# Optimization experiments

Hardware: AMD Instinct MI355X
Metric: run time of the kernel (lower is better)

Reference implementation:

```python
import jax, jax.numpy as jnp
from jax import lax
import numpy as np

B, T, K = 256, 512, 256
MAX_SEQ = 512  # max_sequence_length; output padded to MAX_SEQ + 2


def setup_inputs() -> dict:
    key = jax.random.key(0)
    k1, k2 = jax.random.split(key)
    emissions = jax.random.normal(k1, (B, T, K), dtype=jnp.float32)
    transitions = jax.random.normal(k2, (K, K), dtype=jnp.float32)
    mask = jnp.ones((B, T), dtype=jnp.int32)  # prefix mask; here full-length
    return {"emissions": emissions, "transitions": transitions, "mask": mask,
            "max_sequence_length": MAX_SEQ}


def _crf_decode(emissions, transitions, mask):
    # emissions: [B, T, K] float; transitions: [K, K]; mask: [B, T] int (prefix 1s)
    b, t, k = emissions.shape
    state0 = emissions[:, 0, :]                      # [B, K]
    em_rest = jnp.swapaxes(emissions[:, 1:, :], 0, 1)  # [T-1, B, K]
    mk_rest = jnp.swapaxes(mask[:, 1:], 0, 1)           # [T-1, B]

    def fwd(state, xs):
        em_t, mk_t = xs
        # scores[b, i, j] = state[b, i] + transitions[i, j]  (prev tag i -> cur tag j)
        scores = state[:, :, None] + transitions[None, :, :]   # [B, K, K]
        bp = jnp.argmax(scores, axis=1).astype(jnp.int32)       # [B, K] best prev tag
        new_state = jnp.max(scores, axis=1) + em_t              # [B, K]
        valid = (mk_t > 0)[:, None]
        # RNN-with-mask semantics: keep last valid state past sequence end
        return jnp.where(valid, new_state, state), bp

    last_state, bps = lax.scan(fwd, state0, (em_rest, mk_rest))  # bps: [T-1, B, K]
    last_tag = jnp.argmax(last_state, axis=-1).astype(jnp.int32)  # [B]

    def bwd(tag, xs):
        bp_t, mk_t = xs
        out = tag  # tag at this timestep
        prev = jnp.take_along_axis(bp_t, tag[:, None], axis=1)[:, 0]
        tag = jnp.where(mk_t > 0, prev, tag)  # only step back on valid positions
        return tag, out

    tag0, outs = lax.scan(bwd, last_tag, (bps, mk_rest), reverse=True)
    # outs[t] = tag at position t+1 (t = 0..T-2); tag0 = tag at position 0
    tags = jnp.concatenate([tag0[:, None], jnp.swapaxes(outs, 0, 1)], axis=1)  # [B, T]
    return tags


def reference(emissions, transitions, mask, max_sequence_length):
    tags = _crf_decode(emissions, transitions, mask)
    tags = tags * mask  # zero out padding positions
    pad = max_sequence_length + 2 - tags.shape[1]
    return jnp.pad(tags, ((0, 0), (0, pad)))
```

## Files before the change

kernel.cpp:

```cpp
#include <hip/hip_runtime.h>


#define TK 256
#define TT 512

typedef float v2f __attribute__((ext_vector_type(2)));

__global__ void transpose_kernel(const float* __restrict__ trans,
                                 float* __restrict__ transT) {
  int j = blockIdx.x;
  int i = threadIdx.x;
  transT[(size_t)j * TK + i] = trans[(size_t)i * TK + j];
}

__global__ __launch_bounds__(1024, 4) void crf_fwd(const float* __restrict__ em,
                                                   const float* __restrict__ trans,
                                                   const int* __restrict__ mask,
                                                   float* __restrict__ states) {
  const int b = blockIdx.x;
  const int tid = threadIdx.x;
  const int j = tid & (TK - 1);
  const int h = tid >> 8;

  __shared__ __align__(16) float st[TK];
  __shared__ float part[3 * TK];
  __shared__ int mk[TT];

  v2f tr2[32];
#pragma unroll
  for (int i = 0; i < 32; ++i) {
    tr2[i].x = trans[(size_t)(h * 64 + 2 * i + 0) * TK + j];
    tr2[i].y = trans[(size_t)(h * 64 + 2 * i + 1) * TK + j];
  }

  if (tid < TT) mk[tid] = mask[(size_t)b * TT + tid];

  const size_t base = (size_t)b * TT * TK;
  float cur = 0.f;
  if (h == 0) {
    cur = em[base + j];
    st[j] = cur;
    states[base + j] = cur;
  }
  __syncthreads();

  const float* stp = st + h * 64;
  const float* emp = em + base + TK + j;
  float* outp = states + base + TK + j;

  for (int t = 1; t < TT; ++t) {
    float emv = 0.f;
    if (h == 0) emv = *emp;

    float m0 = -INFINITY, m1 = -INFINITY;
#pragma unroll
    for (int k = 0; k < 16; ++k) {
      const float4 s4 = *reinterpret_cast<const float4*>(stp + 4 * k);
      v2f a = {s4.x, s4.y};
      v2f c = {s4.z, s4.w};
      a = a + tr2[2 * k + 0];
      c = c + tr2[2 * k + 1];
      m0 = fmaxf(fmaxf(m0, a.x), a.y);
      m1 = fmaxf(fmaxf(m1, c.x), c.y);
    }
    const float pm = fmaxf(m0, m1);

    if (h) part[(h - 1) * TK + j] = pm;
    __syncthreads();
    if (h == 0) {
      float m = fmaxf(fmaxf(pm, part[j]),
                      fmaxf(part[TK + j], part[2 * TK + j]));
      float nv = (mk[t] > 0) ? (m + emv) : cur;
      cur = nv;
      st[j] = nv;
      *outp = nv;
      emp += TK;
      outp += TK;
    }
    __syncthreads();
  }
}

__device__ __forceinline__ float wave_max(float m) {
#pragma unroll
  for (int d = 1; d < 64; d <<= 1) m = fmaxf(m, __shfl_xor(m, d, 64));
  return m;
}

__device__ __forceinline__ int first_eq_idx(float s0, float s1, float s2,
                                            float s3, float m) {
  unsigned long long b0 = __ballot(s0 == m);
  unsigned long long b1 = __ballot(s1 == m);
  unsigned long long b2 = __ballot(s2 == m);
  unsigned long long b3 = __ballot(s3 == m);
  int best = 0x7fffffff;
  if (b0) best = min(best, 4 * (__ffsll(b0) - 1) + 0);
  if (b1) best = min(best, 4 * (__ffsll(b1) - 1) + 1);
  if (b2) best = min(best, 4 * (__ffsll(b2) - 1) + 2);
  if (b3) best = min(best, 4 * (__ffsll(b3) - 1) + 3);
  return best;
}

__global__ __launch_bounds__(64, 1) void crf_bwd(const float* __restrict__ states,
                                                 const float* __restrict__ transT,
                                                 const int* __restrict__ mask,
                                                 int* __restrict__ out,
                                                 int out_stride) {
  const int b = blockIdx.x;
  const int lane = threadIdx.x;

  __shared__ int mk[TT];
  for (int q = lane; q < TT; q += 64) mk[q] = mask[(size_t)b * TT + q];
  __syncthreads();

  const size_t sbase = (size_t)b * TT * TK;
  int* outp = out + (size_t)b * out_stride;

  for (int q = TT + lane; q < out_stride; q += 64) outp[q] = 0;

  const float* srow = states + sbase;
  float4 r = *reinterpret_cast<const float4*>(srow + (size_t)(TT - 1) * TK + 4 * lane);
  float lm = fmaxf(fmaxf(r.x, r.y), fmaxf(r.z, r.w));
  lm = wave_max(lm);
  int tag = first_eq_idx(r.x, r.y, r.z, r.w, lm);

  auto LOADROW = [&](int rr) -> float4 {
    return *reinterpret_cast<const float4*>(srow + (size_t)rr * TK + 4 * lane);
  };
  float4 p0 = LOADROW(TT - 2), p1 = LOADROW(TT - 3), p2 = LOADROW(TT - 4),
         p3 = LOADROW(TT - 5);

  auto STEP = [&](float4 pr, int t) {
    int mkt = mk[t];
    if (lane == 0) outp[t] = (mkt > 0) ? tag : 0;
    const float4 tv =
        *reinterpret_cast<const float4*>(transT + (size_t)tag * TK + 4 * lane);
    float s0 = pr.x + tv.x;
    float s1 = pr.y + tv.y;
    float s2 = pr.z + tv.z;
    float s3 = pr.w + tv.w;
    float m = fmaxf(fmaxf(s0, s1), fmaxf(s2, s3));
    m = wave_max(m);
    int prev = first_eq_idx(s0, s1, s2, s3, m);
    tag = (mkt > 0) ? prev : tag;
  };

  int t = TT - 1;
  while (t >= 4) {
    STEP(p0, t);     if (t - 5 >= 0) p0 = LOADROW(t - 5);
    STEP(p1, t - 1); if (t - 6 >= 0) p1 = LOADROW(t - 6);
    STEP(p2, t - 2); if (t - 7 >= 0) p2 = LOADROW(t - 7);
    STEP(p3, t - 3); if (t - 8 >= 0) p3 = LOADROW(t - 8);
    t -= 4;
  }
  STEP(p0, 3);
  STEP(p1, 2);
  STEP(p2, 1);
  if (lane == 0) outp[0] = (mk[0] > 0) ? tag : 0;
}

extern "C" void kernel_launch(void* const* d_in, const int* in_sizes, int n_in,
                              void* d_out, int out_size, void* d_ws, size_t ws_size,
                              hipStream_t stream) {
  const float* em = (const float*)d_in[0];
  const float* trans = (const float*)d_in[1];
  const int* mask = (const int*)d_in[2];
  int* out = (int*)d_out;

  const int B = in_sizes[0] / (TT * TK);
  const int out_stride = out_size / B;

  float* states = (float*)d_ws;
  float* transT = states + (size_t)B * TT * TK;

  transpose_kernel<<<TK, TK, 0, stream>>>(trans, transT);
  crf_fwd<<<B, 1024, 0, stream>>>(em, trans, mask, states);
  crf_bwd<<<B, 64, 0, stream>>>(states, transT, mask, out, out_stride);
}
```

Baseline: 655.9 us.

## Remap forward Viterbi threads to two tags by eight prev-tag groups

The forward kernel now has each thread own two adjacent output tags and a slice of 32 previous tags (8 groups of 128 threads), instead of one tag and 64 previous tags across 4 groups. Each state value loaded from LDS is reused for two output tags, which halves the shared-memory reads per add. The cost is a larger cross-group reduction of 7 partials in thread group 0. The emission for the next step is now prefetched one iteration ahead, to hide global-load latency on the serial recurrence.

```diff
diff --git a/kernel.cpp b/kernel.cpp
--- a/kernel.cpp
+++ b/kernel.cpp
@@ -5,6 +5,7 @@
 #define TT 512
 
 typedef float v2f __attribute__((ext_vector_type(2)));
+typedef float v4f __attribute__((ext_vector_type(4)));
 
 __global__ void transpose_kernel(const float* __restrict__ trans,
                                  float* __restrict__ transT) {
@@ -12,6 +13,11 @@
   int i = threadIdx.x;
   transT[(size_t)j * TK + i] = trans[(size_t)i * TK + j];
 }
+
+#define TR_LIST(X) \
+  X(0) X(1) X(2) X(3) X(4) X(5) X(6) X(7) X(8) X(9) X(10) X(11) X(12) X(13) \
+  X(14) X(15) X(16) X(17) X(18) X(19) X(20) X(21) X(22) X(23) X(24) X(25)   \
+  X(26) X(27) X(28) X(29) X(30) X(31)
 
 __global__ __launch_bounds__(1024, 4) void crf_fwd(const float* __restrict__ em,
                                                    const float* __restrict__ trans,
@@ -19,63 +25,81 @@
                                                    float* __restrict__ states) {
   const int b = blockIdx.x;
   const int tid = threadIdx.x;
-  const int j = tid & (TK - 1);
-  const int h = tid >> 8;
+  const int jp = tid & 127;
+  const int g = tid >> 7;
 
   __shared__ __align__(16) float st[TK];
-  __shared__ float part[3 * TK];
+  __shared__ v2f part[7][128];
   __shared__ int mk[TT];
 
-  v2f tr2[32];
-#pragma unroll
-  for (int i = 0; i < 32; ++i) {
-    tr2[i].x = trans[(size_t)(h * 64 + 2 * i + 0) * TK + j];
-    tr2[i].y = trans[(size_t)(h * 64 + 2 * i + 1) * TK + j];
-  }
+  const float* tb = trans + (size_t)(32 * g) * TK + 2 * jp;
+#define TRDECL(n) const v2f t##n = *reinterpret_cast<const v2f*>(tb + (n) * TK);
+  TR_LIST(TRDECL)
+#undef TRDECL
 
   if (tid < TT) mk[tid] = mask[(size_t)b * TT + tid];
 
   const size_t base = (size_t)b * TT * TK;
-  float cur = 0.f;
-  if (h == 0) {
-    cur = em[base + j];
-    st[j] = cur;
-    states[base + j] = cur;
+  v2f cur = {0.f, 0.f};
+  if (g == 0) {
+    cur = *reinterpret_cast<const v2f*>(em + base + 2 * jp);
+    *reinterpret_cast<v2f*>(st + 2 * jp) = cur;
+    *reinterpret_cast<v2f*>(states + base + 2 * jp) = cur;
   }
   __syncthreads();
 
-  const float* stp = st + h * 64;
-  const float* emp = em + base + TK + j;
-  float* outp = states + base + TK + j;
+  const float* stp = st + 32 * g;
+  const v2f* emp = reinterpret_cast<const v2f*>(em + base + TK) + jp;
+  v2f* outp = reinterpret_cast<v2f*>(states + base + TK) + jp;
+
+  v2f enext = {0.f, 0.f};
+  if (g == 0) enext = *emp;
 
   for (int t = 1; t < TT; ++t) {
-    float emv = 0.f;
-    if (h == 0) emv = *emp;
-
-    float m0 = -INFINITY, m1 = -INFINITY;
+    v2f ecur = enext;
+    if (g == 0 && t + 1 < TT) enext = *(emp + TK / 2);
+
+    float mx = -INFINITY, my = -INFINITY;
+#define STEP4(k, ta, tb_, tc, td)                                        \
+    {                                                                    \
+      const v4f s4 = *reinterpret_cast<const v4f*>(stp + 4 * (k));       \
+      const v2f a0 = ta + (v2f){s4.x, s4.x};                             \
+      const v2f a1 = tb_ + (v2f){s4.y, s4.y};                            \
+      const v2f a2 = tc + (v2f){s4.z, s4.z};                             \
+      const v2f a3 = td + (v2f){s4.w, s4.w};                             \
+      mx = fmaxf(fmaxf(mx, a0.x), a1.x);                                 \
+      my = fmaxf(fmaxf(my, a0.y), a1.y);                                 \
+      mx = fmaxf(fmaxf(mx, a2.x), a3.x);                                 \
+      my = fmaxf(fmaxf(my, a2.y), a3.y);                                 \
+    }
+    STEP4(0, t0, t1, t2, t3)
+    STEP4(1, t4, t5, t6, t7)
+    STEP4(2, t8, t9, t10, t11)
+    STEP4(3, t12, t13, t14, t15)
+    STEP4(4, t16, t17, t18, t19)
+    STEP4(5, t20, t21, t22, t23)
+    STEP4(6, t24, t25, t26, t27)
+    STEP4(7, t28, t29, t30, t31)
+#undef STEP4
+
+    if (g) part[g - 1][jp] = (v2f){mx, my};
+    __syncthreads();
+    if (g == 0) {
 #pragma unroll
-    for (int k = 0; k < 16; ++k) {
-      const float4 s4 = *reinterpret_cast<const float4*>(stp + 4 * k);
-      v2f a = {s4.x, s4.y};
-      v2f c = {s4.z, s4.w};
-      a = a + tr2[2 * k + 0];
-      c = c + tr2[2 * k + 1];
-      m0 = fmaxf(fmaxf(m0, a.x), a.y);
-      m1 = fmaxf(fmaxf(m1, c.x), c.y);
-    }
-    const float pm = fmaxf(m0, m1);
-
-    if (h) part[(h - 1) * TK + j] = pm;
-    __syncthreads();
-    if (h == 0) {
-      float m = fmaxf(fmaxf(pm, part[j]),
-                      fmaxf(part[TK + j], part[2 * TK + j]));
-      float nv = (mk[t] > 0) ? (m + emv) : cur;
+      for (int p = 0; p < 7; ++p) {
+        const v2f q = part[p][jp];
+        mx = fmaxf(mx, q.x);
+        my = fmaxf(my, q.y);
+      }
+      const bool vmask = mk[t] > 0;
+      v2f nv;
+      nv.x = vmask ? mx + ecur.x : cur.x;
+      nv.y = vmask ? my + ecur.y : cur.y;
       cur = nv;
-      st[j] = nv;
+      *reinterpret_cast<v2f*>(st + 2 * jp) = nv;
       *outp = nv;
-      emp += TK;
-      outp += TK;
+      emp += TK / 2;
+      outp += TK / 2;
     }
     __syncthreads();
   }
```

Measured after the change: 665.7 us. About the same (+1.5%).
